# Kernel optimization log

Hardware: AMD Instinct MI355X
Metric: run time of the kernel (lower is better)

Reference implementation:

```python
import jax, jax.numpy as jnp
import numpy as np

K = 64
PI = np.float32(np.pi)


def setup_inputs() -> dict:
    key = jax.random.key(0)
    k1, k2 = jax.random.split(key)
    B, N = 4096, 21
    rotation = jax.random.normal(k1, (B, N, 3, 3), dtype=jnp.float32)
    conditions = jax.random.normal(k2, (B, N, 4 * K), dtype=jnp.float32)
    permute = np.arange(3).astype(np.int64)  # static permutation indices
    return {"rotation": rotation, "conditions": conditions, "permute": permute}


def _mobius_forward(rotation, conditions, p0, p1, p2):
    B, N = rotation.shape[0], rotation.shape[1]
    I3 = jnp.eye(3, dtype=rotation.dtype)

    x = rotation[..., p0]  # [B,N,3]
    y = rotation[..., p1]  # [B,N,3]

    # compute_mcl_parameters_nd
    weights = conditions[..., :K]                      # [B,N,K]
    w = conditions[..., K:].reshape(B, N, K, 3)        # [B,N,K,3]
    proj = I3 - jnp.einsum('bni,bnj->bnij', y, y)      # [B,N,3,3]
    w = jnp.einsum('bnij,bnkj->bnki', proj, w)
    r = -x
    r = r / jnp.linalg.norm(r, axis=-1, keepdims=True)
    v = jnp.cross(y, r)
    v = v / jnp.linalg.norm(v, axis=-1, keepdims=True)
    weights = jax.nn.softplus(weights)
    weights = weights / jnp.sum(weights, axis=-1, keepdims=True)
    w_norm = jnp.linalg.norm(w, axis=-1, keepdims=True)
    w = 0.7 / (1.0 + w_norm) * w

    # _forward_nd
    z = x
    zw = z[:, :, None, :] - w                          # [B,N,K,3]
    zw_norm = jnp.linalg.norm(zw, axis=-1)             # [B,N,K]
    w_norm2 = jnp.sum(w * w, axis=-1)                  # [B,N,K]
    h_z = ((1.0 - w_norm2) / zw_norm ** 2)[..., None] * zw - w  # [B,N,K,3]

    radians = jnp.arctan2(jnp.einsum('bnki,bni->bnk', h_z, v),
                          jnp.einsum('bnki,bni->bnk', h_z, r))
    ang = jnp.where(radians >= 0, radians, radians + 2.0 * PI)
    ang = jnp.sum(weights * ang, axis=2, keepdims=True)          # [B,N,1]
    tx = r * jnp.cos(ang) + v * jnp.sin(ang)                     # [B,N,3]

    zw_unit = zw / zw_norm[..., None]
    theta = jnp.arctan2(jnp.einsum('bni,bni->bn', x, v),
                        jnp.einsum('bni,bni->bn', x, r))[..., None]  # [B,N,1]
    dz_dtheta = -jnp.sin(theta) * r + jnp.cos(theta) * v             # [B,N,3]
    dh_dz = (1.0 - w_norm2)[..., None, None] * (
        I3 - 2.0 * jnp.einsum('bnki,bnkj->bnkij', zw_unit, zw_unit)
    ) / (zw_norm ** 2)[..., None, None]                              # [B,N,K,3,3]
    dh_dtheta = jnp.einsum('bnkpq,bnq->bnkp', dh_dz, dz_dtheta)      # [B,N,K,3]
    dtx = jnp.sum(jnp.linalg.norm(dh_dtheta, axis=-1) * weights, axis=2)  # [B,N]
    ldj = jnp.log(dtx)

    if (p1 - p0 == 1) or (p1 - p0 == -2):
        tz = jnp.cross(tx, y)
    else:
        tz = jnp.cross(y, tx)
    tz = tz / jnp.linalg.norm(tz, axis=-1, keepdims=True)

    cols = [None, None, None]
    cols[p0] = tx
    cols[p1] = y
    cols[p2] = tz
    trotation = jnp.stack(cols, axis=-1)  # [B,N,3,3]
    return trotation, jnp.sum(ldj, axis=-1)


def reference(rotation, conditions, permute):
    p0, p1, p2 = int(permute[0]), int(permute[1]), int(permute[2])
    return _mobius_forward(rotation, conditions, p0, p1, p2)
```

## Files before the change

kernel.cpp:

```cpp
#include <hip/hip_runtime.h>
#include <math.h>

#define PI_F    3.14159265358979323846f
#define TWO_PI  6.28318530717958647692f
#define HALF_PI 1.57079632679489661923f

__device__ __forceinline__ float frcp(float x)  { return __builtin_amdgcn_rcpf(x); }
__device__ __forceinline__ float frsq(float x)  { return __builtin_amdgcn_rsqf(x); }
__device__ __forceinline__ float fsqrt(float x) { return __builtin_amdgcn_sqrtf(x); }

__device__ __forceinline__ void glds16(const void* g, void* l) {
    __builtin_amdgcn_global_load_lds(
        (const __attribute__((address_space(1))) void*)g,
        (__attribute__((address_space(3))) void*)l, 16, 0, 0);
}

__device__ __forceinline__ float fast_atan2_2pi(float y, float x) {
    float ax = fabsf(x), ay = fabsf(y);
    float mx = fmaxf(ax, ay), mn = fminf(ax, ay);
    float a  = (mx > 0.0f) ? mn * frcp(mx) : 0.0f;
    float s  = a * a;
    float r  = fmaf(s, fmaf(s, fmaf(s, fmaf(s, 0.0208351f, -0.085133f),
                                    0.180141f), -0.3302995f), 0.9998660f) * a;
    if (ay > ax) r = HALF_PI - r;
    if (x < 0.0f) r = PI_F - r;
    return (y < 0.0f) ? (TWO_PI - r) : r;
}

struct RotPW { float x0, x1, x2, y0, y1, y2; float4 pw; };

__global__ __launch_bounds__(448)
void mobius_fwd(const float* __restrict__ rot,
                const float* __restrict__ cond,
                const void* __restrict__ perm,
                float* __restrict__ out,
                int B, int N)
{
    const int wave = threadIdx.x >> 6;
    const int lane = threadIdx.x & 63;
    const int sub  = lane >> 4;
    const int j    = lane & 15;
    const int nwav = blockDim.x >> 6;

    const int b0     = blockIdx.x * 4;
    const int nb     = min(4, B - b0);
    const int nit    = N * nb;
    const int nquads = (nit + 3) >> 2;

    const int* pi = (const int*)perm;
    int p0 = pi[0], p1 = pi[1], p2 = pi[2];
    bool pok = ((unsigned)p0 < 3u) && ((unsigned)p1 < 3u) && ((unsigned)p2 < 3u)
               && (p0 != p1) && (p0 != p2) && (p1 != p2);
    if (!pok) {
        const long long* pl = (const long long*)perm;
        p0 = (int)pl[0]; p1 = (int)pl[1]; p2 = (int)pl[2];
    }
    const int dd = p1 - p0;
    const bool swapc = (dd == 1 || dd == -2);

    __shared__ __align__(16) float cbuf[7][2][4][196];
    __shared__ float s_ldj[128];

    const size_t base_item = (size_t)b0 * N;

    auto stage = [&](int par, int qq) {
        if (lane < 48) {
            #pragma unroll
            for (int s = 0; s < 4; ++s) {
                int iv = min(4 * qq + s, nit - 1);
                const float* g = cond + (base_item + iv) * 256 + 64 + 4 * lane;
                glds16(g, &cbuf[wave][par][s][0]);
            }
        }
    };
    auto loadrp = [&](RotPW& d, int qq) {
        int iv = min(4 * qq + sub, nit - 1);
        const float* R = rot + (base_item + iv) * 9;
        d.x0 = R[p0]; d.x1 = R[3 + p0]; d.x2 = R[6 + p0];
        d.y0 = R[p1]; d.y1 = R[3 + p1]; d.y2 = R[6 + p1];
        d.pw = *(const float4*)(cond + (base_item + iv) * 256 + 4 * j);
    };

    RotPW cur{}, nxt{};
    stage(0, wave);
    loadrp(cur, wave);

    int par = 0;
    for (int q = wave; q < nquads; q += nwav, par ^= 1) {
        const int qn = q + nwav;
        const bool have_next = (qn < nquads);

        if (have_next) {
            stage(par ^ 1, qn);
            asm volatile("s_waitcnt vmcnt(4)" ::: "memory");
        } else {
            asm volatile("s_waitcnt vmcnt(0)" ::: "memory");
        }
        __builtin_amdgcn_sched_barrier(0);

        const float* myl = &cbuf[wave][par][sub][12 * j];
        float4 fa = *(const float4*)(myl);
        float4 fb = *(const float4*)(myl + 4);
        float4 fc = *(const float4*)(myl + 8);

        if (have_next) loadrp(nxt, qn);

        const int  i0    = 4 * q + sub;
        const bool valid = (i0 < nit);
        const size_t item = base_item + (valid ? i0 : 0);

        const float x0 = cur.x0, x1 = cur.x1, x2 = cur.x2;
        const float y0 = cur.y0, y1 = cur.y1, y2 = cur.y2;

        float xn2    = x0 * x0 + x1 * x1 + x2 * x2;
        float inv_xn = frsq(xn2);
        float xn     = xn2 * inv_xn;
        float xy     = x0 * y0 + x1 * y1 + x2 * y2;
        float yn2    = y0 * y0 + y1 * y1 + y2 * y2;
        float negA   = yn2 - 2.0f;

        float cv0 = x1 * y2 - x2 * y1;
        float cv1 = x2 * y0 - x0 * y2;
        float cv2 = x0 * y1 - x1 * y0;
        float inv_cn = frsq(cv0 * cv0 + cv1 * cv1 + cv2 * cv2);
        float v0 = cv0 * inv_cn, v1 = cv1 * inv_cn, v2 = cv2 * inv_cn;

        float PW[4] = {cur.pw.x, cur.pw.y, cur.pw.z, cur.pw.w};
        float W0[4] = {fa.x, fa.w, fb.z, fc.y};
        float W1[4] = {fa.y, fb.x, fb.w, fc.z};
        float W2[4] = {fa.z, fb.y, fc.x, fc.w};

        float pp = 0.0f, pa = 0.0f, pd = 0.0f;
        #pragma unroll
        for (int cc = 0; cc < 4; ++cc) {
            float w0 = W0[cc], w1 = W1[cc], w2 = W2[cc];
            float yw  = y0 * w0 + y1 * w1 + y2 * w2;
            float wp2 = w0 * w0 + w1 * w1 + w2 * w2;
            float xwp = x0 * w0 + x1 * w1 + x2 * w2;
            float vwp = v0 * w0 + v1 * w1 + v2 * w2;
            float qn2 = fmaxf(fmaf(yw * yw, negA, wp2), 0.0f);
            float sc  = 0.7f * frcp(1.0f + fsqrt(qn2));
            float wn2 = (sc * sc) * qn2;
            float xw  = sc * fmaf(-xy, yw, xwp);
            float zwn2 = fmaf(-2.0f, xw, xn2 + wn2);
            float c   = (1.0f - wn2) * frcp(zwn2);
            float cp1 = c + 1.0f;
            float hv  = -(cp1 * (sc * vwp));
            float hr  = fmaf(cp1, xw * inv_xn, -(c * xn));
            float ang = fast_atan2_2pi(hv, hr);
            float p   = __logf(1.0f + __expf(PW[cc]));
            pp += p; pa = fmaf(p, ang, pa); pd = fmaf(p, c, pd);
        }

        #pragma unroll
        for (int off = 8; off >= 1; off >>= 1) {
            pp += __shfl_xor(pp, off, 64);
            pa += __shfl_xor(pa, off, 64);
            pd += __shfl_xor(pd, off, 64);
        }

        float ip   = frcp(pp);
        float angT = pa * ip;
        float ldj  = __logf(pd * ip);

        float sa, ca;
        __sincosf(angT, &sa, &ca);
        float r0 = -x0 * inv_xn, r1 = -x1 * inv_xn, r2 = -x2 * inv_xn;
        float t0 = fmaf(r0, ca, v0 * sa);
        float t1 = fmaf(r1, ca, v1 * sa);
        float t2 = fmaf(r2, ca, v2 * sa);

        float u0, u1, u2;
        if (swapc) {
            u0 = t1 * y2 - t2 * y1;
            u1 = t2 * y0 - t0 * y2;
            u2 = t0 * y1 - t1 * y0;
        } else {
            u0 = y1 * t2 - y2 * t1;
            u1 = y2 * t0 - y0 * t2;
            u2 = y0 * t1 - y1 * t0;
        }
        float iun = frsq(u0 * u0 + u1 * u1 + u2 * u2);
        u0 *= iun; u1 *= iun; u2 *= iun;

        if (valid) {
            if (j < 9) {
                int row = (j >= 6) ? 2 : (j >= 3) ? 1 : 0;
                int cp  = j - 3 * row;
                float tr = (row == 0) ? t0 : (row == 1) ? t1 : t2;
                float yr = (row == 0) ? y0 : (row == 1) ? y1 : y2;
                float ur = (row == 0) ? u0 : (row == 1) ? u1 : u2;
                float val = (cp == p0) ? tr : (cp == p1) ? yr : ur;
                out[item * 9 + j] = val;
            }
            if (j == 0) s_ldj[i0] = ldj;
        }

        cur = nxt;
    }

    __syncthreads();
    if (threadIdx.x < nb) {
        float acc = 0.0f;
        for (int n = 0; n < N; ++n) acc += s_ldj[threadIdx.x * N + n];
        out[(size_t)B * N * 9 + b0 + threadIdx.x] = acc;
    }
}

extern "C" void kernel_launch(void* const* d_in, const int* in_sizes, int n_in,
                              void* d_out, int out_size, void* d_ws, size_t ws_size,
                              hipStream_t stream) {
    const float* rot  = (const float*)d_in[0];
    const float* cond = (const float*)d_in[1];
    const void*  perm = d_in[2];
    float* out = (float*)d_out;

    int items = in_sizes[0] / 9;
    int B = out_size - items * 9;
    int N = items / B;

    int grid = (B + 3) / 4;
    mobius_fwd<<<dim3(grid), dim3(448), 0, stream>>>(rot, cond, perm, out, B, N);
}
```

Measured before the change: 30.44 us.

## Drop register prefetch of rotation/weights and emit outputs from one lane

Removes the software-pipelined register prefetch of rotation columns and softplus weights for the next quad and loads them at the top of each iteration instead, issued before the LDS stage of the next quad. The epilogue (sincos, cross product, normalisation and output write) now runs only in lane j==0 of each 16-lane group, which writes all nine output entries itself rather than spreading them across nine lanes. This cuts register pressure and redundant epilogue work, but it exposes global-load latency each iteration and replaces coalesced stores with scattered stores from a single lane.

```diff
diff --git a/kernel.cpp b/kernel.cpp
--- a/kernel.cpp
+++ b/kernel.cpp
@@ -26,8 +26,6 @@
     if (x < 0.0f) r = PI_F - r;
     return (y < 0.0f) ? (TWO_PI - r) : r;
 }
-
-struct RotPW { float x0, x1, x2, y0, y1, y2; float4 pw; };
 
 __global__ __launch_bounds__(448)
 void mobius_fwd(const float* __restrict__ rot,
@@ -73,44 +71,36 @@
             }
         }
     };
-    auto loadrp = [&](RotPW& d, int qq) {
-        int iv = min(4 * qq + sub, nit - 1);
-        const float* R = rot + (base_item + iv) * 9;
-        d.x0 = R[p0]; d.x1 = R[3 + p0]; d.x2 = R[6 + p0];
-        d.y0 = R[p1]; d.y1 = R[3 + p1]; d.y2 = R[6 + p1];
-        d.pw = *(const float4*)(cond + (base_item + iv) * 256 + 4 * j);
-    };
-
-    RotPW cur{}, nxt{};
+
     stage(0, wave);
-    loadrp(cur, wave);
 
     int par = 0;
     for (int q = wave; q < nquads; q += nwav, par ^= 1) {
+        const int  i0    = 4 * q + sub;
+        const bool valid = (i0 < nit);
+        const size_t item = base_item + (valid ? i0 : 0);
+
+        const float* C = cond + item * 256;
+        float4 pw4 = *(const float4*)(C + 4 * j);
+        const float* R = rot + item * 9;
+        float x0 = R[p0], x1 = R[3 + p0], x2 = R[6 + p0];
+        float y0 = R[p1], y1 = R[3 + p1], y2 = R[6 + p1];
+
+        asm volatile("" ::: "memory");
+
         const int qn = q + nwav;
         const bool have_next = (qn < nquads);
-
         if (have_next) {
             stage(par ^ 1, qn);
             asm volatile("s_waitcnt vmcnt(4)" ::: "memory");
         } else {
             asm volatile("s_waitcnt vmcnt(0)" ::: "memory");
         }
-        __builtin_amdgcn_sched_barrier(0);
 
         const float* myl = &cbuf[wave][par][sub][12 * j];
         float4 fa = *(const float4*)(myl);
         float4 fb = *(const float4*)(myl + 4);
         float4 fc = *(const float4*)(myl + 8);
-
-        if (have_next) loadrp(nxt, qn);
-
-        const int  i0    = 4 * q + sub;
-        const bool valid = (i0 < nit);
-        const size_t item = base_item + (valid ? i0 : 0);
-
-        const float x0 = cur.x0, x1 = cur.x1, x2 = cur.x2;
-        const float y0 = cur.y0, y1 = cur.y1, y2 = cur.y2;
 
         float xn2    = x0 * x0 + x1 * x1 + x2 * x2;
         float inv_xn = frsq(xn2);
@@ -125,7 +115,7 @@
         float inv_cn = frsq(cv0 * cv0 + cv1 * cv1 + cv2 * cv2);
         float v0 = cv0 * inv_cn, v1 = cv1 * inv_cn, v2 = cv2 * inv_cn;
 
-        float PW[4] = {cur.pw.x, cur.pw.y, cur.pw.z, cur.pw.w};
+        float PW[4] = {pw4.x, pw4.y, pw4.z, pw4.w};
         float W0[4] = {fa.x, fa.w, fb.z, fc.y};
         float W1[4] = {fa.y, fb.x, fb.w, fc.z};
         float W2[4] = {fa.z, fb.y, fc.x, fc.w};
@@ -159,44 +149,38 @@
             pd += __shfl_xor(pd, off, 64);
         }
 
-        float ip   = frcp(pp);
-        float angT = pa * ip;
-        float ldj  = __logf(pd * ip);
-
-        float sa, ca;
-        __sincosf(angT, &sa, &ca);
-        float r0 = -x0 * inv_xn, r1 = -x1 * inv_xn, r2 = -x2 * inv_xn;
-        float t0 = fmaf(r0, ca, v0 * sa);
-        float t1 = fmaf(r1, ca, v1 * sa);
-        float t2 = fmaf(r2, ca, v2 * sa);
-
-        float u0, u1, u2;
-        if (swapc) {
-            u0 = t1 * y2 - t2 * y1;
-            u1 = t2 * y0 - t0 * y2;
-            u2 = t0 * y1 - t1 * y0;
-        } else {
-            u0 = y1 * t2 - y2 * t1;
-            u1 = y2 * t0 - y0 * t2;
-            u2 = y0 * t1 - y1 * t0;
-        }
-        float iun = frsq(u0 * u0 + u1 * u1 + u2 * u2);
-        u0 *= iun; u1 *= iun; u2 *= iun;
-
-        if (valid) {
-            if (j < 9) {
-                int row = (j >= 6) ? 2 : (j >= 3) ? 1 : 0;
-                int cp  = j - 3 * row;
-                float tr = (row == 0) ? t0 : (row == 1) ? t1 : t2;
-                float yr = (row == 0) ? y0 : (row == 1) ? y1 : y2;
-                float ur = (row == 0) ? u0 : (row == 1) ? u1 : u2;
-                float val = (cp == p0) ? tr : (cp == p1) ? yr : ur;
-                out[item * 9 + j] = val;
+        if (j == 0 && valid) {
+            float ip   = frcp(pp);
+            float angT = pa * ip;
+            float ldj  = __logf(pd * ip);
+
+            float sa, ca;
+            __sincosf(angT, &sa, &ca);
+            float r0 = -x0 * inv_xn, r1 = -x1 * inv_xn, r2 = -x2 * inv_xn;
+            float t0 = fmaf(r0, ca, v0 * sa);
+            float t1 = fmaf(r1, ca, v1 * sa);
+            float t2 = fmaf(r2, ca, v2 * sa);
+
+            float u0, u1, u2;
+            if (swapc) {
+                u0 = t1 * y2 - t2 * y1;
+                u1 = t2 * y0 - t0 * y2;
+                u2 = t0 * y1 - t1 * y0;
+            } else {
+                u0 = y1 * t2 - y2 * t1;
+                u1 = y2 * t0 - y0 * t2;
+                u2 = y0 * t1 - y1 * t0;
             }
-            if (j == 0) s_ldj[i0] = ldj;
-        }
-
-        cur = nxt;
+            float iun = frsq(u0 * u0 + u1 * u1 + u2 * u2);
+            u0 *= iun; u1 *= iun; u2 *= iun;
+
+            float* T = out + item * 9;
+            T[p0] = t0; T[3 + p0] = t1; T[6 + p0] = t2;
+            T[p1] = y0; T[3 + p1] = y1; T[6 + p1] = y2;
+            T[p2] = u0; T[3 + p2] = u1; T[6 + p2] = u2;
+
+            s_ldj[i0] = ldj;
+        }
     }
 
     __syncthreads();
```

Result: no change. 30.10 us (-1.1%).
